# Performance work log

Hardware: AMD Instinct MI355X
Metric: run time of the kernel (lower is better)

## Reference

```python
import jax, jax.numpy as jnp
import numpy as np
import math

D_MODEL = 1024
RPN_D = 256
SUP_HW = 20  # support feature map is 20x20 -> 400 tokens


def _positional_encoding(max_len, d_model):
    pos = np.arange(max_len, dtype=np.float32)[:, None]
    div = np.exp(np.arange(0, d_model, 2, dtype=np.float32) * -(math.log(10000.0) / float(d_model)))
    pe = np.zeros((max_len, d_model), dtype=np.float32)
    pe[:, 0::2] = np.sin(pos * div)
    pe[:, 1::2] = np.cos(pos * div)
    return jnp.asarray(pe)


def setup_inputs() -> dict:
    key = jax.random.key(0)
    ks = jax.random.split(key, 6)
    B, S, H = 4, 5, 4
    fh, fw = 64, 64
    base_feat = jax.random.normal(ks[0], (B, D_MODEL, fh, fw), dtype=jnp.float32)
    support_feat = jax.random.normal(ks[1], (B, S, D_MODEL, SUP_HW, SUP_HW), dtype=jnp.float32)
    Qw = jax.random.normal(ks[2], (H, RPN_D, D_MODEL), dtype=jnp.float32) * 0.01
    Qb = jnp.zeros((H, RPN_D), dtype=jnp.float32)
    Kw = jax.random.normal(ks[3], (H, RPN_D, D_MODEL), dtype=jnp.float32) * 0.01
    Kb = jnp.zeros((H, RPN_D), dtype=jnp.float32)
    Mw = jax.random.normal(ks[4], (D_MODEL, H * D_MODEL), dtype=jnp.float32) * 0.02
    Mb = jnp.zeros((D_MODEL,), dtype=jnp.float32)
    return {"base_feat": base_feat, "support_feat": support_feat,
            "Qw": Qw, "Qb": Qb, "Kw": Kw, "Kb": Kb, "Mw": Mw, "Mb": Mb}


def reference(base_feat, support_feat, Qw, Qb, Kw, Kb, Mw, Mb):
    B, C, fh, fw = base_feat.shape
    S = support_feat.shape[1]
    H = Qw.shape[0]
    Lq = fh * fw
    Lk = SUP_HW * SUP_HW

    # support_mat: [S, B, Lk, C]  (transpose(0,1) then flatten spatial, then transpose)
    support_mat = jnp.transpose(support_feat, (1, 0, 2, 3, 4)).reshape(S, B, C, Lk)
    support_mat = jnp.transpose(support_mat, (0, 1, 3, 2))
    # query_mat: [B, Lq, C]
    query_mat = jnp.transpose(base_feat.reshape(B, C, Lq), (0, 2, 1))

    pe = _positional_encoding(400, D_MODEL)[:Lk]  # [Lk, C]
    s_mat = support_mat + pe[None, None]          # [S, B, Lk, C]

    # per-head projections (q is independent of shot, compute once)
    q = jnp.einsum('blc,hdc->hbld', query_mat, Qw) + Qb[:, None, None, :]   # [H,B,Lq,d]
    k = jnp.einsum('sbkc,hdc->hsbkd', s_mat, Kw) + Kb[:, None, None, None, :]  # [H,S,B,Lk,d]

    scores = jnp.einsum('hbld,hsbkd->hsblk', q, k) / math.sqrt(RPN_D)  # [H,S,B,Lq,Lk]
    attn = jax.nn.softmax(scores, axis=-1)
    z = jnp.einsum('hsblk,sbkc->hsblc', attn, s_mat)  # [H,S,B,Lq,C]

    # shot_mode == 'mean'
    z = jnp.mean(z, axis=1)  # [H,B,Lq,C]

    # concat heads along feature dim (head order preserved): [B,Lq,H*C]
    att = jnp.transpose(z, (1, 2, 0, 3)).reshape(B, Lq, H * C)
    att = jax.nn.relu(att @ Mw.T + Mb)  # [B,Lq,C]

    att = jnp.transpose(att, (0, 2, 1)).reshape(B, C, fh, fw)
    # attention_type == 'product'
    correlation_feat = base_feat * att
    return correlation_feat
```

## Files before the change

kernel.cpp:

```cpp
#include <hip/hip_runtime.h>
#include <stdint.h>

#define DEVI __device__ __forceinline__

typedef __attribute__((ext_vector_type(8))) short bf16x8;
typedef __attribute__((ext_vector_type(4))) float f32x4;
typedef __attribute__((ext_vector_type(4))) unsigned short us4;
typedef unsigned short u16;

constexpr int B_ = 4, S_ = 5, H_ = 4, C_ = 1024, D_ = 256;
constexpr int LQ = 4096, LK = 400, LKP = 448;

DEVI u16 f2b(float f){
  uint32_t x = __float_as_uint(f);
  uint32_t r = (x + 0x7FFFu + ((x >> 16) & 1u)) >> 16;
  return (u16)r;
}

typedef __attribute__((address_space(1))) const void ASG;
typedef __attribute__((address_space(3))) void ASL;
DEVI void gload16(const void* g, void* l){
  __builtin_amdgcn_global_load_lds((ASG*)g, (ASL*)l, 16, 0, 0);
}

__global__ __launch_bounds__(256) void k_cvt(const float* __restrict__ s, u16* __restrict__ d, int n4){
  int i = blockIdx.x*256 + threadIdx.x;
  if (i >= n4) return;
  float4 v = ((const float4*)s)[i];
  us4 o; o.x = f2b(v.x); o.y = f2b(v.y); o.z = f2b(v.z); o.w = f2b(v.w);
  *(us4*)(d + (size_t)i*4) = o;
}

__global__ __launch_bounds__(256) void k_transpose_x(const float* __restrict__ base, u16* __restrict__ Xb){
  __shared__ float t[32][33];
  int l0 = blockIdx.x*32, c0 = blockIdx.y*32, b = blockIdx.z;
  int tx = threadIdx.x & 31, ty = threadIdx.x >> 5;
  const float* src = base + ((size_t)b*C_ + c0)*LQ + l0;
  #pragma unroll
  for (int i=0;i<4;i++){ int cc = ty + i*8; t[cc][tx] = src[(size_t)cc*LQ + tx]; }
  __syncthreads();
  u16* dst = Xb + ((size_t)b*LQ + l0)*C_ + c0;
  #pragma unroll
  for (int i=0;i<4;i++){ int ll = ty + i*8; dst[(size_t)ll*C_ + tx] = f2b(t[tx][ll]); }
}

__global__ __launch_bounds__(256) void k_build_smat(const float* __restrict__ sup, u16* __restrict__ kc){
  __shared__ float t[32][33];
  int p0 = blockIdx.x*32, c0 = blockIdx.y*32;
  int s = blockIdx.z / B_, b = blockIdx.z % B_;
  int tx = threadIdx.x & 31, ty = threadIdx.x >> 5;
  const float* src = sup + ((size_t)(b*S_ + s)*C_ + c0)*LK + p0;
  #pragma unroll
  for (int i=0;i<4;i++){
    int cc = ty + i*8;
    int p = p0 + tx;
    int c = c0 + cc;
    float v = 0.f;
    if (p < LK){
      v = src[(size_t)cc*LK + tx];
      float dv = expf(-(float)(c & ~1) * (9.210340371976184f / 1024.f));
      float arg = (float)p * dv;
      v += (c & 1) ? cosf(arg) : sinf(arg);
    }
    t[cc][tx] = v;
  }
  __syncthreads();
  u16* dkc = kc + ((size_t)((s*B_ + b)*LKP + p0))*C_ + c0;
  #pragma unroll
  for (int i=0;i<4;i++){ int pp = ty + i*8; dkc[(size_t)pp*C_ + tx] = f2b(t[tx][pp]); }
}

DEVI void stage_half(const u16* P, int64_t ld, u16* dst, int wid, int r8, int s8){
  #pragma unroll
  for (int it=0; it<2; ++it){
    int ck = wid + it*8;
    gload16(P + (size_t)(ck*8 + r8)*ld + s8*8, dst + ck*512);
  }
}
DEVI bf16x8 ldsread(const u16* base, int row, int kk, int lane){
  int sl = ((kk<<2) + (lane>>4)) ^ (row & 7);
  return *(const bf16x8*)&base[row*64 + sl*8];
}

template<int CEPI, bool FIRST, bool FINAL, bool BIAS>
__global__ __launch_bounds__(512,1) void k8(
    const u16* __restrict__ A, const u16* __restrict__ Bm, void* __restrict__ Cm,
    const float* __restrict__ bias, const float* __restrict__ basep, const float* __restrict__ Mb,
    int tilesM, int64_t lda, int64_t ldb, int64_t ldc,
    int spc, int NT, int64_t aChunk, int64_t bChunk,
    int bdiv, int64_t aS0, int64_t aS1, int64_t bS0, int64_t bS1,
    int64_t cS0, int64_t cS1, int biasS0, float scale, int Nmax, int Mmax, int swz){
  __shared__ __align__(16) u16 lds[2][2][16384];
  int tid = threadIdx.x, lane = tid & 63, wid = tid >> 6;
  int bx = blockIdx.x;
  int mt, ntile;
  if (swz == 2){ int x = bx & 7, j = bx >> 3; mt = 2*x + (j >> 2); ntile = j & 3; }
  else {
    if (swz == 1) bx = (bx & 7) * (gridDim.x >> 3) + (bx >> 3);
    mt = bx % tilesM; ntile = bx / tilesM;
  }
  int z = blockIdx.y, i0 = z / bdiv, i1 = z % bdiv;
  const u16* Ab = A + i0*aS0 + i1*aS1 + (size_t)mt*256*lda;
  const u16* Bb = Bm + i0*bS0 + i1*bS1 + (size_t)ntile*256*ldb;
  int r8 = lane >> 3, s8 = (lane & 7) ^ r8;
  int wr = wid >> 2, wc = wid & 3;

  f32x4 acc[8][4];
  #pragma unroll
  for (int i=0;i<8;i++)
    #pragma unroll
    for (int j=0;j<4;j++) acc[i][j] = (f32x4){0.f,0.f,0.f,0.f};

  const u16 *ApS = Ab, *BpS = Bb; int cs = 0;
  stage_half(ApS,                   lda, &lds[0][0][0],    wid, r8, s8);
  stage_half(ApS + (size_t)128*lda, lda, &lds[0][0][8192], wid, r8, s8);
  stage_half(BpS,                   ldb, &lds[0][1][0],    wid, r8, s8);
  stage_half(BpS + (size_t)128*ldb, ldb, &lds[0][1][8192], wid, r8, s8);
  ApS += 64; BpS += 64;
  if (++cs == spc){ cs = 0; ApS += aChunk - (int64_t)spc*64; BpS += bChunk - (int64_t)spc*64; }

  for (int t = 0; t < NT; ++t){
    int cur = t & 1, nxt = cur ^ 1;
    bool pf = (t + 1 < NT);
    const u16* lA = &lds[cur][0][0];
    const u16* lB = &lds[cur][1][0];
    if (pf){
      u16* sA = &lds[nxt][0][0];
      u16* sB = &lds[nxt][1][0];
      stage_half(ApS,                   lda, sA,        wid, r8, s8);
      stage_half(ApS + (size_t)128*lda, lda, sA + 8192, wid, r8, s8);
      stage_half(BpS,                   ldb, sB,        wid, r8, s8);
      stage_half(BpS + (size_t)128*ldb, ldb, sB + 8192, wid, r8, s8);
      ApS += 64; BpS += 64;
      if (++cs == spc){ cs = 0; ApS += aChunk - (int64_t)spc*64; BpS += bChunk - (int64_t)spc*64; }
      asm volatile("s_waitcnt vmcnt(8)" ::: "memory");
    } else {
      asm volatile("s_waitcnt vmcnt(0)" ::: "memory");
    }
    asm volatile("s_barrier" ::: "memory");

    bf16x8 bfr[4][2];
    #pragma unroll
    for (int jn=0;jn<4;jn++)
      #pragma unroll
      for (int kk=0;kk<2;kk++)
        bfr[jn][kk] = ldsread(lB, wc*64 + jn*16 + (lane & 15), kk, lane);

    #pragma unroll
    for (int p = 0; p < 4; ++p){
      bf16x8 af[2][2];
      #pragma unroll
      for (int dm=0;dm<2;dm++)
        #pragma unroll
        for (int kk=0;kk<2;kk++)
          af[dm][kk] = ldsread(lA, wr*128 + (p*2+dm)*16 + (lane & 15), kk, lane);
      __builtin_amdgcn_s_setprio(1);
      #pragma unroll
      for (int dm=0;dm<2;dm++)
        #pragma unroll
        for (int jn=0;jn<4;jn++)
          #pragma unroll
          for (int kk=0;kk<2;kk++)
            acc[p*2+dm][jn] = __builtin_amdgcn_mfma_f32_16x16x32_bf16(af[dm][kk], bfr[jn][kk], acc[p*2+dm][jn], 0,0,0);
      __builtin_amdgcn_s_setprio(0);
    }
    asm volatile("s_barrier" ::: "memory");
  }

  int g = lane >> 4, c16 = lane & 15;
  if constexpr (CEPI == 0){
    u16* Cb = (u16*)Cm + i0*cS0 + i1*cS1;
    #pragma unroll
    for (int jn=0;jn<4;jn++){
      int n = ntile*256 + wc*64 + jn*16 + c16;
      if (n >= Nmax) continue;
      float bv = 0.f;
      if (BIAS) bv = bias[(size_t)i0*biasS0 + n];
      #pragma unroll
      for (int im=0;im<8;im++){
        int m = mt*256 + wr*128 + im*16 + g*4;
        if (m >= Mmax) continue;
        #pragma unroll
        for (int r=0;r<4;r++)
          Cb[(size_t)(m + r)*ldc + n] = f2b((acc[im][jn][r] + bv)*scale);
      }
    }
  } else {
    float* Cb = (float*)Cm + i0*cS0 + i1*cS1;
    const float* Bs = basep + i0*cS0 + i1*cS1;
    #pragma unroll
    for (int jn=0;jn<4;jn++){
      int n = ntile*256 + wc*64 + jn*16 + c16;
      float mbv = 0.f;
      if (FINAL) mbv = Mb[n];
      #pragma unroll
      for (int im=0;im<8;im++){
        int m = mt*256 + wr*128 + im*16 + g*4;
        float* p = Cb + (size_t)n*ldc + m;
        float4 v;
        v.x = acc[im][jn][0]; v.y = acc[im][jn][1]; v.z = acc[im][jn][2]; v.w = acc[im][jn][3];
        if (!FIRST){
          float4 old = *(const float4*)p;
          v.x += old.x; v.y += old.y; v.z += old.z; v.w += old.w;
        }
        if (FINAL){
          float4 bs = *(const float4*)(Bs + (size_t)n*ldc + m);
          v.x = bs.x * fmaxf(0.2f*v.x + mbv, 0.f);
          v.y = bs.y * fmaxf(0.2f*v.y + mbv, 0.f);
          v.z = bs.z * fmaxf(0.2f*v.z + mbv, 0.f);
          v.w = bs.w * fmaxf(0.2f*v.w + mbv, 0.f);
        }
        *(float4*)p = v;
      }
    }
  }
}

__global__ __launch_bounds__(512) void k_scores(
    const u16* __restrict__ qws, const u16* __restrict__ kws,
    u16* __restrict__ attn, int h0){
  __shared__ __align__(16) u16 lQ[128*64];
  __shared__ __align__(16) u16 lK[400*64];
  int tid = threadIdx.x, lane = tid & 63, wid = tid >> 6;
  int m0 = blockIdx.x * 128;
  int b = blockIdx.y;
  int zz = blockIdx.z;
  int s = zz % 5, h = h0 + zz / 5;
  const u16* Qp = qws + ((size_t)(h*B_ + b)*LQ + m0)*D_;
  const u16* Kp = kws + ((size_t)((h*S_ + s)*B_ + b))*((size_t)LKP*D_);
  int r8 = lane >> 3, s8 = (lane & 7) ^ r8;
  f32x4 acc[25];
  #pragma unroll
  for (int t=0;t<25;t++) acc[t] = (f32x4){0.f,0.f,0.f,0.f};
  int wm = wid * 16;
  for (int k0 = 0; k0 < 256; k0 += 64){
    __syncthreads();
    #pragma unroll
    for (int c = 0; c < 2; ++c){
      int cc = wid + c*8;
      int row = cc*8 + r8;
      gload16(Qp + (size_t)row*D_ + k0 + s8*8, &lQ[cc*512]);
    }
    for (int cc = wid; cc < 50; cc += 8){
      int row = cc*8 + r8;
      gload16(Kp + (size_t)row*D_ + k0 + s8*8, &lK[cc*512]);
    }
    __syncthreads();
    #pragma unroll
    for (int kk = 0; kk < 2; ++kk){
      int rowA = wm + (lane & 15);
      int slA = ((kk<<2) + (lane>>4)) ^ (rowA & 7);
      bf16x8 af = *(const bf16x8*)&lQ[rowA*64 + slA*8];
      #pragma unroll
      for (int t=0;t<25;t++){
        int rowB = t*16 + (lane & 15);
        int slB = ((kk<<2) + (lane>>4)) ^ (rowB & 7);
        bf16x8 bf = *(const bf16x8*)&lK[rowB*64 + slB*8];
        acc[t] = __builtin_amdgcn_mfma_f32_16x16x32_bf16(af, bf, acc[t], 0,0,0);
      }
    }
  }
  float mx[4] = {-1e30f,-1e30f,-1e30f,-1e30f};
  #pragma unroll
  for (int t=0;t<25;t++)
    #pragma unroll
    for (int r=0;r<4;r++) mx[r] = fmaxf(mx[r], acc[t][r]);
  #pragma unroll
  for (int r=0;r<4;r++){
    mx[r] = fmaxf(mx[r], __shfl_xor(mx[r], 1));
    mx[r] = fmaxf(mx[r], __shfl_xor(mx[r], 2));
    mx[r] = fmaxf(mx[r], __shfl_xor(mx[r], 4));
    mx[r] = fmaxf(mx[r], __shfl_xor(mx[r], 8));
  }
  float sm[4] = {0.f,0.f,0.f,0.f};
  #pragma unroll
  for (int t=0;t<25;t++)
    #pragma unroll
    for (int r=0;r<4;r++){ float e = __expf(acc[t][r] - mx[r]); acc[t][r] = e; sm[r] += e; }
  #pragma unroll
  for (int r=0;r<4;r++){
    sm[r] += __shfl_xor(sm[r], 1);
    sm[r] += __shfl_xor(sm[r], 2);
    sm[r] += __shfl_xor(sm[r], 4);
    sm[r] += __shfl_xor(sm[r], 8);
    sm[r] = 1.f / sm[r];
  }
  u16* ap = attn + ((size_t)((zz*B_ + b)*LQ) + m0 + wm)*LKP;
  int g = lane >> 4, c16 = lane & 15;
  #pragma unroll
  for (int t=0;t<25;t++)
    #pragma unroll
    for (int r=0;r<4;r++)
      ap[(size_t)(g*4 + r)*LKP + t*16 + c16] = f2b(acc[t][r] * sm[r]);
  for (int t = lane; t < 16*48; t += 64){
    int rr = t / 48, cp = 400 + (t % 48);
    ap[(size_t)rr*LKP + cp] = 0;
  }
}

extern "C" void kernel_launch(void* const* d_in, const int* in_sizes, int n_in,
                              void* d_out, int out_size, void* d_ws, size_t ws_size,
                              hipStream_t stream){
  const float* base = (const float*)d_in[0];
  const float* sup  = (const float*)d_in[1];
  const float* Qw   = (const float*)d_in[2];
  const float* Qb   = (const float*)d_in[3];
  const float* Kw   = (const float*)d_in[4];
  const float* Kb   = (const float*)d_in[5];
  const float* Mw   = (const float*)d_in[6];
  const float* Mb   = (const float*)d_in[7];
  float* out = (float*)d_out;
  char* ws = (char*)d_ws;

  u16* wQw = (u16*)(ws + 0);
  u16* wKw = (u16*)(ws + 2097152);
  u16* wMw = (u16*)(ws + 4194304);
  u16* wKC = (u16*)(ws + 12582912);
  u16* wK  = (u16*)(ws + 30932992);
  u16* wQ  = (u16*)(ws + 49283072);
  u16* wVt = (u16*)(ws + 82837504);

  const int GH = (ws_size >= 266338304ull) ? 2 : 1;
  const int NG = H_ / GH;
  u16* wAT = (u16*)(ws + 82837504 + (size_t)GH*18350080ull);
  u16* wXb = wAT;

  const int BIG = 1 << 30;

  k_cvt<<<1024, 256, 0, stream>>>(Qw, wQw, 262144);
  k_cvt<<<1024, 256, 0, stream>>>(Kw, wKw, 262144);
  k_cvt<<<4096, 256, 0, stream>>>(Mw, wMw, 1048576);
  k_transpose_x<<<dim3(128, 32, 4), 256, 0, stream>>>(base, wXb);
  k_build_smat<<<dim3(14, 32, 20), 256, 0, stream>>>(sup, wKC);

  k8<0,false,false,true><<<dim3(2, 80), 512, 0, stream>>>(
      wKC, wKw, wK, Kb, nullptr, nullptr,
      2, C_, C_, D_, 16, 16, 1024, 1024,
      20, 0, (int64_t)LKP*C_, (int64_t)D_*C_, 0,
      (int64_t)S_*B_*LKP*D_, (int64_t)LKP*D_, D_, 1.f, BIG, LKP, 0);

  k8<0,false,false,true><<<dim3(16, 16), 512, 0, stream>>>(
      wXb, wQw, wQ, Qb, nullptr, nullptr,
      16, C_, C_, D_, 16, 16, 1024, 1024,
      4, 0, (int64_t)LQ*C_, (int64_t)D_*C_, 0,
      (int64_t)B_*LQ*D_, (int64_t)LQ*D_, D_, 1.f/16.f, BIG, BIG, 1);

  for (int g = 0; g < NG; ++g){
    k8<0,false,false,false><<<dim3(8, GH*20), 512, 0, stream>>>(
        wMw + (size_t)(g*GH)*C_, wKC, wVt, nullptr, nullptr, nullptr,
        4, (int64_t)H_*C_, C_, LKP, 16, 16, 1024, 1024,
        20, (int64_t)C_, 0, 0, (int64_t)LKP*C_,
        (int64_t)20*C_*LKP, (int64_t)C_*LKP, 0, 1.f, LKP, BIG, 0);

    k_scores<<<dim3(32, 4, GH*5), 512, 0, stream>>>(wQ, wK, wAT, g*GH);

    if (g == 0){
      k8<1,true,false,false><<<dim3(64, 4), 512, 0, stream>>>(
          wAT, wVt, out, nullptr, base, Mb,
          16, LKP, LKP, LQ, 7, GH*35, (int64_t)B_*LQ*LKP, (int64_t)B_*C_*LKP,
          1, (int64_t)LQ*LKP, 0, (int64_t)C_*LKP, 0,
          (int64_t)C_*LQ, 0, 0, 1.f, BIG, BIG, 2);
    } else if (g == NG - 1){
      k8<1,false,true,false><<<dim3(64, 4), 512, 0, stream>>>(
          wAT, wVt, out, nullptr, base, Mb,
          16, LKP, LKP, LQ, 7, GH*35, (int64_t)B_*LQ*LKP, (int64_t)B_*C_*LKP,
          1, (int64_t)LQ*LKP, 0, (int64_t)C_*LKP, 0,
          (int64_t)C_*LQ, 0, 0, 1.f, BIG, BIG, 2);
    } else {
      k8<1,false,false,false><<<dim3(64, 4), 512, 0, stream>>>(
          wAT, wVt, out, nullptr, base, Mb,
          16, LKP, LKP, LQ, 7, GH*35, (int64_t)B_*LQ*LKP, (int64_t)B_*C_*LKP,
          1, (int64_t)LQ*LKP, 0, (int64_t)C_*LKP, 0,
          (int64_t)C_*LQ, 0, 0, 1.f, BIG, BIG, 2);
    }
  }
}
```

Baseline: 758.9 us.

## Pack attention/V along a dense KV axis, add dedicated attn-V GEMM kernel

The attention and V matrices are now packed densely along a combined shot/head KV axis (GH*5*400 rounded up to 64) instead of per-shot 448-padded chunks. This removes the chunk-stride logic and the wasted padded K-steps in the attn·V GEMM. A new k8d kernel handles that GEMM with 128x256 tiles, triple-buffered A staging and a fused residual/ReLU/product epilogue. k_scores is restructured so 8 waves split rows and KV columns, with Q read directly from global, double-buffered K in LDS and a cross-wave softmax sum through LDS. It also drops the max subtraction in softmax, which relies on scores staying small enough that exp does not overflow.

```diff
diff --git a/kernel.cpp b/kernel.cpp
--- a/kernel.cpp
+++ b/kernel.cpp
@@ -82,26 +82,23 @@
   return *(const bf16x8*)&base[row*64 + sl*8];
 }
 
-template<int CEPI, bool FIRST, bool FINAL, bool BIAS>
+template<int CEPI, bool BIAS>
 __global__ __launch_bounds__(512,1) void k8(
     const u16* __restrict__ A, const u16* __restrict__ Bm, void* __restrict__ Cm,
-    const float* __restrict__ bias, const float* __restrict__ basep, const float* __restrict__ Mb,
-    int tilesM, int64_t lda, int64_t ldb, int64_t ldc,
-    int spc, int NT, int64_t aChunk, int64_t bChunk,
+    const float* __restrict__ bias,
+    int tilesM, int64_t lda, int64_t ldb, int64_t ldc, int NT,
     int bdiv, int64_t aS0, int64_t aS1, int64_t bS0, int64_t bS1,
-    int64_t cS0, int64_t cS1, int biasS0, float scale, int Nmax, int Mmax, int swz){
+    int64_t cS0, int64_t cS1, int64_t aZ, int64_t bZ, int64_t cZ,
+    int biasS0, float scale, int Nmax, int Mmax, int swz){
   __shared__ __align__(16) u16 lds[2][2][16384];
   int tid = threadIdx.x, lane = tid & 63, wid = tid >> 6;
   int bx = blockIdx.x;
-  int mt, ntile;
-  if (swz == 2){ int x = bx & 7, j = bx >> 3; mt = 2*x + (j >> 2); ntile = j & 3; }
-  else {
-    if (swz == 1) bx = (bx & 7) * (gridDim.x >> 3) + (bx >> 3);
-    mt = bx % tilesM; ntile = bx / tilesM;
-  }
+  if (swz == 1) bx = (bx & 7) * (gridDim.x >> 3) + (bx >> 3);
+  int mt = bx % tilesM, ntile = bx / tilesM;
   int z = blockIdx.y, i0 = z / bdiv, i1 = z % bdiv;
-  const u16* Ab = A + i0*aS0 + i1*aS1 + (size_t)mt*256*lda;
-  const u16* Bb = Bm + i0*bS0 + i1*bS1 + (size_t)ntile*256*ldb;
+  int iz = blockIdx.z;
+  const u16* Ab = A + i0*aS0 + i1*aS1 + iz*aZ + (size_t)mt*256*lda;
+  const u16* Bb = Bm + i0*bS0 + i1*bS1 + iz*bZ + (size_t)ntile*256*ldb;
   int r8 = lane >> 3, s8 = (lane & 7) ^ r8;
   int wr = wid >> 2, wc = wid & 3;
 
@@ -111,13 +108,12 @@
     #pragma unroll
     for (int j=0;j<4;j++) acc[i][j] = (f32x4){0.f,0.f,0.f,0.f};
 
-  const u16 *ApS = Ab, *BpS = Bb; int cs = 0;
+  const u16 *ApS = Ab, *BpS = Bb;
   stage_half(ApS,                   lda, &lds[0][0][0],    wid, r8, s8);
   stage_half(ApS + (size_t)128*lda, lda, &lds[0][0][8192], wid, r8, s8);
   stage_half(BpS,                   ldb, &lds[0][1][0],    wid, r8, s8);
   stage_half(BpS + (size_t)128*ldb, ldb, &lds[0][1][8192], wid, r8, s8);
   ApS += 64; BpS += 64;
-  if (++cs == spc){ cs = 0; ApS += aChunk - (int64_t)spc*64; BpS += bChunk - (int64_t)spc*64; }
 
   for (int t = 0; t < NT; ++t){
     int cur = t & 1, nxt = cur ^ 1;
@@ -132,7 +128,6 @@
       stage_half(BpS,                   ldb, sB,        wid, r8, s8);
       stage_half(BpS + (size_t)128*ldb, ldb, sB + 8192, wid, r8, s8);
       ApS += 64; BpS += 64;
-      if (++cs == spc){ cs = 0; ApS += aChunk - (int64_t)spc*64; BpS += bChunk - (int64_t)spc*64; }
       asm volatile("s_waitcnt vmcnt(8)" ::: "memory");
     } else {
       asm volatile("s_waitcnt vmcnt(0)" ::: "memory");
@@ -168,59 +163,134 @@
   }
 
   int g = lane >> 4, c16 = lane & 15;
-  if constexpr (CEPI == 0){
-    u16* Cb = (u16*)Cm + i0*cS0 + i1*cS1;
-    #pragma unroll
-    for (int jn=0;jn<4;jn++){
-      int n = ntile*256 + wc*64 + jn*16 + c16;
-      if (n >= Nmax) continue;
-      float bv = 0.f;
-      if (BIAS) bv = bias[(size_t)i0*biasS0 + n];
-      #pragma unroll
-      for (int im=0;im<8;im++){
-        int m = mt*256 + wr*128 + im*16 + g*4;
-        if (m >= Mmax) continue;
+  u16* Cb = (u16*)Cm + i0*cS0 + i1*cS1 + iz*cZ;
+  #pragma unroll
+  for (int jn=0;jn<4;jn++){
+    int n = ntile*256 + wc*64 + jn*16 + c16;
+    if (n >= Nmax) continue;
+    float bv = 0.f;
+    if (BIAS) bv = bias[(size_t)i0*biasS0 + n];
+    #pragma unroll
+    for (int im=0;im<8;im++){
+      int m = mt*256 + wr*128 + im*16 + g*4;
+      if (m >= Mmax) continue;
+      #pragma unroll
+      for (int r=0;r<4;r++)
+        Cb[(size_t)(m + r)*ldc + n] = f2b((acc[im][jn][r] + bv)*scale);
+    }
+  }
+}
+
+template<bool FIRST, bool FINAL>
+__global__ __launch_bounds__(512,1) void k8d(
+    const u16* __restrict__ A, const u16* __restrict__ Bm, float* __restrict__ Cm,
+    const float* __restrict__ basep, const float* __restrict__ Mb,
+    int KVP, int NT){
+  __shared__ __align__(16) u16 lA[3][8192];
+  __shared__ __align__(16) u16 lB[2][16384];
+  int tid = threadIdx.x, lane = tid & 63, wid = tid >> 6;
+  int x = blockIdx.x & 7, jj = blockIdx.x >> 3;
+  int mt = x*4 + (jj >> 2), nt = jj & 3;
+  int b = blockIdx.y;
+  const u16* Ab = A + ((size_t)b*LQ + (size_t)mt*128)*KVP;
+  const u16* Bb = Bm + ((size_t)b*C_ + (size_t)nt*256)*KVP;
+  int r8 = lane >> 3, s8 = (lane & 7) ^ r8;
+  int wr = wid >> 2, wc = wid & 3;
+
+  f32x4 acc[4][4];
+  #pragma unroll
+  for (int i=0;i<4;i++)
+    #pragma unroll
+    for (int j=0;j<4;j++) acc[i][j] = (f32x4){0.f,0.f,0.f,0.f};
+
+  const u16 *Bp = Bb, *Ap = Ab;
+  stage_half(Bp,                   KVP, lB[0],        wid, r8, s8);
+  stage_half(Bp + (size_t)128*KVP, KVP, lB[0] + 8192, wid, r8, s8);
+  Bp += 64;
+  stage_half(Ap, KVP, lA[0], wid, r8, s8); Ap += 64;
+  stage_half(Ap, KVP, lA[1], wid, r8, s8); Ap += 64;
+
+  int ia = 0, ia2 = 2, ib = 0;
+  for (int t = 0; t < NT; ++t){
+    const u16* lAc = lA[ia];
+    const u16* lBc = lB[ib];
+    if (t + 1 < NT){
+      u16* dB = lB[ib ^ 1];
+      stage_half(Bp,                   KVP, dB,        wid, r8, s8);
+      stage_half(Bp + (size_t)128*KVP, KVP, dB + 8192, wid, r8, s8);
+      Bp += 64;
+    }
+    if (t + 2 < NT){
+      stage_half(Ap, KVP, lA[ia2], wid, r8, s8);
+      Ap += 64;
+    }
+    if (t + 2 < NT)      asm volatile("s_waitcnt vmcnt(8)" ::: "memory");
+    else if (t + 1 < NT) asm volatile("s_waitcnt vmcnt(6)" ::: "memory");
+    else                 asm volatile("s_waitcnt vmcnt(0)" ::: "memory");
+    asm volatile("s_barrier" ::: "memory");
+
+    bf16x8 bfr[4][2], af[4][2];
+    #pragma unroll
+    for (int jn=0;jn<4;jn++)
+      #pragma unroll
+      for (int kk=0;kk<2;kk++)
+        bfr[jn][kk] = ldsread(lBc, wc*64 + jn*16 + (lane & 15), kk, lane);
+    #pragma unroll
+    for (int im=0;im<4;im++)
+      #pragma unroll
+      for (int kk=0;kk<2;kk++)
+        af[im][kk] = ldsread(lAc, wr*64 + im*16 + (lane & 15), kk, lane);
+    __builtin_amdgcn_s_setprio(1);
+    #pragma unroll
+    for (int im=0;im<4;im++)
+      #pragma unroll
+      for (int jn=0;jn<4;jn++)
         #pragma unroll
-        for (int r=0;r<4;r++)
-          Cb[(size_t)(m + r)*ldc + n] = f2b((acc[im][jn][r] + bv)*scale);
-      }
-    }
-  } else {
-    float* Cb = (float*)Cm + i0*cS0 + i1*cS1;
-    const float* Bs = basep + i0*cS0 + i1*cS1;
-    #pragma unroll
-    for (int jn=0;jn<4;jn++){
-      int n = ntile*256 + wc*64 + jn*16 + c16;
-      float mbv = 0.f;
-      if (FINAL) mbv = Mb[n];
-      #pragma unroll
-      for (int im=0;im<8;im++){
-        int m = mt*256 + wr*128 + im*16 + g*4;
-        float* p = Cb + (size_t)n*ldc + m;
-        float4 v;
-        v.x = acc[im][jn][0]; v.y = acc[im][jn][1]; v.z = acc[im][jn][2]; v.w = acc[im][jn][3];
-        if (!FIRST){
-          float4 old = *(const float4*)p;
-          v.x += old.x; v.y += old.y; v.z += old.z; v.w += old.w;
-        }
-        if (FINAL){
-          float4 bs = *(const float4*)(Bs + (size_t)n*ldc + m);
-          v.x = bs.x * fmaxf(0.2f*v.x + mbv, 0.f);
-          v.y = bs.y * fmaxf(0.2f*v.y + mbv, 0.f);
-          v.z = bs.z * fmaxf(0.2f*v.z + mbv, 0.f);
-          v.w = bs.w * fmaxf(0.2f*v.w + mbv, 0.f);
-        }
-        *(float4*)p = v;
-      }
+        for (int kk=0;kk<2;kk++)
+          acc[im][jn] = __builtin_amdgcn_mfma_f32_16x16x32_bf16(af[im][kk], bfr[jn][kk], acc[im][jn], 0,0,0);
+    __builtin_amdgcn_s_setprio(0);
+    asm volatile("s_barrier" ::: "memory");
+    ia = (ia + 1 == 3) ? 0 : ia + 1;
+    ia2 = (ia2 + 1 == 3) ? 0 : ia2 + 1;
+    ib ^= 1;
+  }
+
+  int g = lane >> 4, c16 = lane & 15;
+  float* Cb = Cm + (size_t)b*C_*LQ;
+  const float* Bs = basep + (size_t)b*C_*LQ;
+  #pragma unroll
+  for (int jn=0;jn<4;jn++){
+    int n = nt*256 + wc*64 + jn*16 + c16;
+    float mbv = 0.f;
+    if (FINAL) mbv = Mb[n];
+    #pragma unroll
+    for (int im=0;im<4;im++){
+      int m = mt*128 + wr*64 + im*16 + g*4;
+      float* p = Cb + (size_t)n*LQ + m;
+      float4 v;
+      v.x = acc[im][jn][0]; v.y = acc[im][jn][1]; v.z = acc[im][jn][2]; v.w = acc[im][jn][3];
+      if (!FIRST){
+        float4 old = *(const float4*)p;
+        v.x += old.x; v.y += old.y; v.z += old.z; v.w += old.w;
+      }
+      if (FINAL){
+        float4 bs = *(const float4*)(Bs + (size_t)n*LQ + m);
+        v.x = bs.x * fmaxf(0.2f*v.x + mbv, 0.f);
+        v.y = bs.y * fmaxf(0.2f*v.y + mbv, 0.f);
+        v.z = bs.z * fmaxf(0.2f*v.z + mbv, 0.f);
+        v.w = bs.w * fmaxf(0.2f*v.w + mbv, 0.f);
+      }
+      *(float4*)p = v;
     }
   }
 }
 
 __global__ __launch_bounds__(512) void k_scores(
     const u16* __restrict__ qws, const u16* __restrict__ kws,
-    u16* __restrict__ attn, int h0){
-  __shared__ __align__(16) u16 lQ[128*64];
-  __shared__ __align__(16) u16 lK[400*64];
+    u16* __restrict__ attn, int h0, int KVP, int padw, int nz){
+  __shared__ __align__(16) u16 lK[2][448*64];
+  __shared__ float red[128][4];
+  __shared__ float rsum[128];
   int tid = threadIdx.x, lane = tid & 63, wid = tid >> 6;
   int m0 = blockIdx.x * 128;
   int b = blockIdx.y;
@@ -229,72 +299,110 @@
   const u16* Qp = qws + ((size_t)(h*B_ + b)*LQ + m0)*D_;
   const u16* Kp = kws + ((size_t)((h*S_ + s)*B_ + b))*((size_t)LKP*D_);
   int r8 = lane >> 3, s8 = (lane & 7) ^ r8;
-  f32x4 acc[25];
-  #pragma unroll
-  for (int t=0;t<25;t++) acc[t] = (f32x4){0.f,0.f,0.f,0.f};
-  int wm = wid * 16;
-  for (int k0 = 0; k0 < 256; k0 += 64){
-    __syncthreads();
-    #pragma unroll
-    for (int c = 0; c < 2; ++c){
-      int cc = wid + c*8;
-      int row = cc*8 + r8;
-      gload16(Qp + (size_t)row*D_ + k0 + s8*8, &lQ[cc*512]);
-    }
-    for (int cc = wid; cc < 50; cc += 8){
-      int row = cc*8 + r8;
-      gload16(Kp + (size_t)row*D_ + k0 + s8*8, &lK[cc*512]);
-    }
-    __syncthreads();
-    #pragma unroll
-    for (int kk = 0; kk < 2; ++kk){
-      int rowA = wm + (lane & 15);
-      int slA = ((kk<<2) + (lane>>4)) ^ (rowA & 7);
-      bf16x8 af = *(const bf16x8*)&lQ[rowA*64 + slA*8];
-      #pragma unroll
-      for (int t=0;t<25;t++){
-        int rowB = t*16 + (lane & 15);
-        int slB = ((kk<<2) + (lane>>4)) ^ (rowB & 7);
-        bf16x8 bf = *(const bf16x8*)&lK[rowB*64 + slB*8];
-        acc[t] = __builtin_amdgcn_mfma_f32_16x16x32_bf16(af, bf, acc[t], 0,0,0);
-      }
-    }
-  }
-  float mx[4] = {-1e30f,-1e30f,-1e30f,-1e30f};
-  #pragma unroll
-  for (int t=0;t<25;t++)
-    #pragma unroll
-    for (int r=0;r<4;r++) mx[r] = fmaxf(mx[r], acc[t][r]);
-  #pragma unroll
-  for (int r=0;r<4;r++){
-    mx[r] = fmaxf(mx[r], __shfl_xor(mx[r], 1));
-    mx[r] = fmaxf(mx[r], __shfl_xor(mx[r], 2));
-    mx[r] = fmaxf(mx[r], __shfl_xor(mx[r], 4));
-    mx[r] = fmaxf(mx[r], __shfl_xor(mx[r], 8));
-  }
-  float sm[4] = {0.f,0.f,0.f,0.f};
-  #pragma unroll
-  for (int t=0;t<25;t++)
-    #pragma unroll
-    for (int r=0;r<4;r++){ float e = __expf(acc[t][r] - mx[r]); acc[t][r] = e; sm[r] += e; }
-  #pragma unroll
-  for (int r=0;r<4;r++){
-    sm[r] += __shfl_xor(sm[r], 1);
-    sm[r] += __shfl_xor(sm[r], 2);
-    sm[r] += __shfl_xor(sm[r], 4);
-    sm[r] += __shfl_xor(sm[r], 8);
-    sm[r] = 1.f / sm[r];
-  }
-  u16* ap = attn + ((size_t)((zz*B_ + b)*LQ) + m0 + wm)*LKP;
-  int g = lane >> 4, c16 = lane & 15;
-  #pragma unroll
-  for (int t=0;t<25;t++)
-    #pragma unroll
-    for (int r=0;r<4;r++)
-      ap[(size_t)(g*4 + r)*LKP + t*16 + c16] = f2b(acc[t][r] * sm[r]);
-  for (int t = lane; t < 16*48; t += 64){
-    int rr = t / 48, cp = 400 + (t % 48);
-    ap[(size_t)rr*LKP + cp] = 0;
+  int c16 = lane & 15, g = lane >> 4;
+  int wm2 = wid >> 2, wkv = wid & 3;
+
+  f32x4 acc[4][7];
+  #pragma unroll
+  for (int m=0;m<4;m++)
+    #pragma unroll
+    for (int t=0;t<7;t++) acc[m][t] = (f32x4){0.f,0.f,0.f,0.f};
+
+  #pragma unroll
+  for (int i=0;i<7;i++){
+    int ck = wid + i*8;
+    gload16(Kp + (size_t)(ck*8 + r8)*D_ + s8*8, &lK[0][ck*512]);
+  }
+
+  for (int t = 0; t < 4; ++t){
+    int k0 = t*64;
+    bf16x8 af[4][2];
+    #pragma unroll
+    for (int m=0;m<4;m++)
+      #pragma unroll
+      for (int kk=0;kk<2;kk++){
+        int row = wm2*64 + m*16 + c16;
+        af[m][kk] = *(const bf16x8*)(Qp + (size_t)row*D_ + k0 + kk*32 + g*8);
+      }
+    if (t + 1 < 4){
+      #pragma unroll
+      for (int i=0;i<7;i++){
+        int ck = wid + i*8;
+        gload16(Kp + (size_t)(ck*8 + r8)*D_ + (k0 + 64) + s8*8, &lK[(t+1)&1][ck*512]);
+      }
+      asm volatile("s_waitcnt vmcnt(15)" ::: "memory");
+    } else {
+      asm volatile("s_waitcnt vmcnt(8)" ::: "memory");
+    }
+    asm volatile("s_barrier" ::: "memory");
+    const u16* lKc = &lK[t & 1][0];
+    __builtin_amdgcn_s_setprio(1);
+    #pragma unroll
+    for (int tt=0;tt<7;tt++)
+      #pragma unroll
+      for (int kk=0;kk<2;kk++){
+        bf16x8 bf = ldsread(lKc, wkv*112 + tt*16 + c16, kk, lane);
+        #pragma unroll
+        for (int m=0;m<4;m++)
+          acc[m][tt] = __builtin_amdgcn_mfma_f32_16x16x32_bf16(af[m][kk], bf, acc[m][tt], 0,0,0);
+      }
+    __builtin_amdgcn_s_setprio(0);
+    asm volatile("s_barrier" ::: "memory");
+  }
+
+  int tmax = (wkv == 3) ? 4 : 7;
+  float psum[4][4];
+  #pragma unroll
+  for (int m=0;m<4;m++)
+    #pragma unroll
+    for (int r=0;r<4;r++) psum[m][r] = 0.f;
+  for (int tt=0; tt<tmax; ++tt)
+    #pragma unroll
+    for (int m=0;m<4;m++)
+      #pragma unroll
+      for (int r=0;r<4;r++){
+        float e = __expf(acc[m][tt][r]);
+        acc[m][tt][r] = e;
+        psum[m][r] += e;
+      }
+  #pragma unroll
+  for (int m=0;m<4;m++)
+    #pragma unroll
+    for (int r=0;r<4;r++){
+      psum[m][r] += __shfl_xor(psum[m][r], 1);
+      psum[m][r] += __shfl_xor(psum[m][r], 2);
+      psum[m][r] += __shfl_xor(psum[m][r], 4);
+      psum[m][r] += __shfl_xor(psum[m][r], 8);
+    }
+  if (c16 == 0){
+    #pragma unroll
+    for (int m=0;m<4;m++)
+      #pragma unroll
+      for (int r=0;r<4;r++)
+        red[wm2*64 + m*16 + g*4 + r][wkv] = psum[m][r];
+  }
+  __syncthreads();
+  if (tid < 128) rsum[tid] = 1.f / (red[tid][0] + red[tid][1] + red[tid][2] + red[tid][3]);
+  __syncthreads();
+
+  u16* ap = attn + ((size_t)b*LQ + m0)*KVP + (size_t)zz*400;
+  for (int m=0;m<4;m++)
+    #pragma unroll
+    for (int r=0;r<4;r++){
+      int rowl = wm2*64 + m*16 + g*4 + r;
+      float rs = rsum[rowl];
+      for (int tt=0; tt<tmax; ++tt){
+        int col = wkv*112 + tt*16 + c16;
+        ap[(size_t)rowl*KVP + col] = f2b(acc[m][tt][r] * rs);
+      }
+    }
+  if (zz == nz - 1 && padw > 0){
+    u16* base2 = attn + ((size_t)b*LQ + m0)*KVP + (KVP - padw);
+    int total = 128 * padw;
+    for (int i = tid; i < total; i += 512){
+      int rr = i / padw, cc = i % padw;
+      base2[(size_t)rr*KVP + cc] = 0;
+    }
   }
 }
 
@@ -312,6 +420,13 @@
   float* out = (float*)d_out;
   char* ws = (char*)d_ws;
 
+  const int GH = (ws_size >= 247988224ull) ? 2 : 1;
+  const int NG = H_ / GH;
+  const int NZ = GH * 5;
+  const int KVP = (NZ*400 + 63) & ~63;
+  const int NT = KVP / 64;
+  const int PADW = KVP - NZ*400;
+
   u16* wQw = (u16*)(ws + 0);
   u16* wKw = (u16*)(ws + 2097152);
   u16* wMw = (u16*)(ws + 4194304);
@@ -319,10 +434,7 @@
   u16* wK  = (u16*)(ws + 30932992);
   u16* wQ  = (u16*)(ws + 49283072);
   u16* wVt = (u16*)(ws + 82837504);
-
-  const int GH = (ws_size >= 266338304ull) ? 2 : 1;
-  const int NG = H_ / GH;
-  u16* wAT = (u16*)(ws + 82837504 + (size_t)GH*18350080ull);
+  u16* wAT = (u16*)(ws + 82837504 + (size_t)B_*C_*KVP*2);
   u16* wXb = wAT;
 
   const int BIG = 1 << 30;
@@ -333,45 +445,36 @@
   k_transpose_x<<<dim3(128, 32, 4), 256, 0, stream>>>(base, wXb);
   k_build_smat<<<dim3(14, 32, 20), 256, 0, stream>>>(sup, wKC);
 
-  k8<0,false,false,true><<<dim3(2, 80), 512, 0, stream>>>(
-      wKC, wKw, wK, Kb, nullptr, nullptr,
-      2, C_, C_, D_, 16, 16, 1024, 1024,
+  k8<0,true><<<dim3(2, 80, 1), 512, 0, stream>>>(
+      wKC, wKw, wK, Kb,
+      2, C_, C_, D_, 16,
       20, 0, (int64_t)LKP*C_, (int64_t)D_*C_, 0,
-      (int64_t)S_*B_*LKP*D_, (int64_t)LKP*D_, D_, 1.f, BIG, LKP, 0);
-
-  k8<0,false,false,true><<<dim3(16, 16), 512, 0, stream>>>(
-      wXb, wQw, wQ, Qb, nullptr, nullptr,
-      16, C_, C_, D_, 16, 16, 1024, 1024,
+      (int64_t)S_*B_*LKP*D_, (int64_t)LKP*D_, 0, 0, 0,
+      D_, 1.f, BIG, LKP, 0);
+
+  k8<0,true><<<dim3(16, 16, 1), 512, 0, stream>>>(
+      wXb, wQw, wQ, Qb,
+      16, C_, C_, D_, 16,
       4, 0, (int64_t)LQ*C_, (int64_t)D_*C_, 0,
-      (int64_t)B_*LQ*D_, (int64_t)LQ*D_, D_, 1.f/16.f, BIG, BIG, 1);
+      (int64_t)B_*LQ*D_, (int64_t)LQ*D_, 0, 0, 0,
+      D_, 1.f/16.f, BIG, BIG, 1);
 
   for (int g = 0; g < NG; ++g){
-    k8<0,false,false,false><<<dim3(8, GH*20), 512, 0, stream>>>(
-        wMw + (size_t)(g*GH)*C_, wKC, wVt, nullptr, nullptr, nullptr,
-        4, (int64_t)H_*C_, C_, LKP, 16, 16, 1024, 1024,
-        20, (int64_t)C_, 0, 0, (int64_t)LKP*C_,
-        (int64_t)20*C_*LKP, (int64_t)C_*LKP, 0, 1.f, LKP, BIG, 0);
-
-    k_scores<<<dim3(32, 4, GH*5), 512, 0, stream>>>(wQ, wK, wAT, g*GH);
-
-    if (g == 0){
-      k8<1,true,false,false><<<dim3(64, 4), 512, 0, stream>>>(
-          wAT, wVt, out, nullptr, base, Mb,
-          16, LKP, LKP, LQ, 7, GH*35, (int64_t)B_*LQ*LKP, (int64_t)B_*C_*LKP,
-          1, (int64_t)LQ*LKP, 0, (int64_t)C_*LKP, 0,
-          (int64_t)C_*LQ, 0, 0, 1.f, BIG, BIG, 2);
+    k8<0,false><<<dim3(8, NZ, 4), 512, 0, stream>>>(
+        wMw + (size_t)(g*GH)*C_, wKC, wVt, nullptr,
+        4, (int64_t)H_*C_, C_, KVP, 16,
+        5, (int64_t)C_, 0, 0, (int64_t)B_*LKP*C_,
+        2000, 400, 0, (int64_t)LKP*C_, (int64_t)C_*KVP,
+        0, 1.f, 400, BIG, 0);
+
+    k_scores<<<dim3(32, 4, NZ), 512, 0, stream>>>(wQ, wK, wAT, g*GH, KVP, PADW, NZ);
+
+    if (g == 0 && NG > 1){
+      k8d<true,false><<<dim3(128, 4), 512, 0, stream>>>(wAT, wVt, out, base, Mb, KVP, NT);
     } else if (g == NG - 1){
-      k8<1,false,true,false><<<dim3(64, 4), 512, 0, stream>>>(
-          wAT, wVt, out, nullptr, base, Mb,
-          16, LKP, LKP, LQ, 7, GH*35, (int64_t)B_*LQ*LKP, (int64_t)B_*C_*LKP,
-          1, (int64_t)LQ*LKP, 0, (int64_t)C_*LKP, 0,
-          (int64_t)C_*LQ, 0, 0, 1.f, BIG, BIG, 2);
+      k8d<false,true><<<dim3(128, 4), 512, 0, stream>>>(wAT, wVt, out, base, Mb, KVP, NT);
     } else {
-      k8<1,false,false,false><<<dim3(64, 4), 512, 0, stream>>>(
-          wAT, wVt, out, nullptr, base, Mb,
-          16, LKP, LKP, LQ, 7, GH*35, (int64_t)B_*LQ*LKP, (int64_t)B_*C_*LKP,
-          1, (int64_t)LQ*LKP, 0, (int64_t)C_*LKP, 0,
-          (int64_t)C_*LQ, 0, 0, 1.f, BIG, BIG, 2);
-    }
-  }
-}
+      k8d<false,false><<<dim3(128, 4), 512, 0, stream>>>(wAT, wVt, out, base, Mb, KVP, NT);
+    }
+  }
+}
```

Measured after the change: 1.960 ms. 158% more time.

## Pack shot/head attention chunks contiguously along K and stagger B-tile prefetch

Applied to the files above, without the earlier changes.

Attention probabilities and the V^T matrix now place all shots and heads of a group contiguously along the reduction dimension, padded once to a multiple of 64 instead of padding each 400-wide chunk to 448. This removes the per-chunk pointer jumps in the GEMM and cuts wasted padded K iterations, so the big attn×V GEMM does less work. The B-operand prefetch is also split and issued between MFMA phases to overlap loads with compute, with the wait count adjusted. Risks are wait-count correctness with the staggered loads, and if NG is 1 the first-pass epilogue path changes.

```diff
diff --git a/kernel.cpp b/kernel.cpp
--- a/kernel.cpp
+++ b/kernel.cpp
@@ -86,10 +86,10 @@
 __global__ __launch_bounds__(512,1) void k8(
     const u16* __restrict__ A, const u16* __restrict__ Bm, void* __restrict__ Cm,
     const float* __restrict__ bias, const float* __restrict__ basep, const float* __restrict__ Mb,
-    int tilesM, int64_t lda, int64_t ldb, int64_t ldc,
-    int spc, int NT, int64_t aChunk, int64_t bChunk,
+    int tilesM, int64_t lda, int64_t ldb, int64_t ldc, int NT,
     int bdiv, int64_t aS0, int64_t aS1, int64_t bS0, int64_t bS1,
-    int64_t cS0, int64_t cS1, int biasS0, float scale, int Nmax, int Mmax, int swz){
+    int64_t cS0, int64_t cS1, int64_t aZ, int64_t bZ, int64_t cZ,
+    int biasS0, float scale, int Nmax, int Mmax, int swz){
   __shared__ __align__(16) u16 lds[2][2][16384];
   int tid = threadIdx.x, lane = tid & 63, wid = tid >> 6;
   int bx = blockIdx.x;
@@ -100,8 +100,9 @@
     mt = bx % tilesM; ntile = bx / tilesM;
   }
   int z = blockIdx.y, i0 = z / bdiv, i1 = z % bdiv;
-  const u16* Ab = A + i0*aS0 + i1*aS1 + (size_t)mt*256*lda;
-  const u16* Bb = Bm + i0*bS0 + i1*bS1 + (size_t)ntile*256*ldb;
+  int iz = blockIdx.z;
+  const u16* Ab = A + i0*aS0 + i1*aS1 + iz*aZ + (size_t)mt*256*lda;
+  const u16* Bb = Bm + i0*bS0 + i1*bS1 + iz*bZ + (size_t)ntile*256*ldb;
   int r8 = lane >> 3, s8 = (lane & 7) ^ r8;
   int wr = wid >> 2, wc = wid & 3;
 
@@ -111,29 +112,24 @@
     #pragma unroll
     for (int j=0;j<4;j++) acc[i][j] = (f32x4){0.f,0.f,0.f,0.f};
 
-  const u16 *ApS = Ab, *BpS = Bb; int cs = 0;
+  const u16 *ApS = Ab, *BpS = Bb;
   stage_half(ApS,                   lda, &lds[0][0][0],    wid, r8, s8);
   stage_half(ApS + (size_t)128*lda, lda, &lds[0][0][8192], wid, r8, s8);
   stage_half(BpS,                   ldb, &lds[0][1][0],    wid, r8, s8);
   stage_half(BpS + (size_t)128*ldb, ldb, &lds[0][1][8192], wid, r8, s8);
   ApS += 64; BpS += 64;
-  if (++cs == spc){ cs = 0; ApS += aChunk - (int64_t)spc*64; BpS += bChunk - (int64_t)spc*64; }
 
   for (int t = 0; t < NT; ++t){
     int cur = t & 1, nxt = cur ^ 1;
     bool pf = (t + 1 < NT);
     const u16* lA = &lds[cur][0][0];
     const u16* lB = &lds[cur][1][0];
+    u16* sA = &lds[nxt][0][0];
+    u16* sB = &lds[nxt][1][0];
     if (pf){
-      u16* sA = &lds[nxt][0][0];
-      u16* sB = &lds[nxt][1][0];
       stage_half(ApS,                   lda, sA,        wid, r8, s8);
       stage_half(ApS + (size_t)128*lda, lda, sA + 8192, wid, r8, s8);
-      stage_half(BpS,                   ldb, sB,        wid, r8, s8);
-      stage_half(BpS + (size_t)128*ldb, ldb, sB + 8192, wid, r8, s8);
-      ApS += 64; BpS += 64;
-      if (++cs == spc){ cs = 0; ApS += aChunk - (int64_t)spc*64; BpS += bChunk - (int64_t)spc*64; }
-      asm volatile("s_waitcnt vmcnt(8)" ::: "memory");
+      asm volatile("s_waitcnt vmcnt(4)" ::: "memory");
     } else {
       asm volatile("s_waitcnt vmcnt(0)" ::: "memory");
     }
@@ -163,13 +159,16 @@
           for (int kk=0;kk<2;kk++)
             acc[p*2+dm][jn] = __builtin_amdgcn_mfma_f32_16x16x32_bf16(af[dm][kk], bfr[jn][kk], acc[p*2+dm][jn], 0,0,0);
       __builtin_amdgcn_s_setprio(0);
+      if (p == 0 && pf) stage_half(BpS,                   ldb, sB,        wid, r8, s8);
+      if (p == 1 && pf) stage_half(BpS + (size_t)128*ldb, ldb, sB + 8192, wid, r8, s8);
     }
     asm volatile("s_barrier" ::: "memory");
+    if (pf){ ApS += 64; BpS += 64; }
   }
 
   int g = lane >> 4, c16 = lane & 15;
   if constexpr (CEPI == 0){
-    u16* Cb = (u16*)Cm + i0*cS0 + i1*cS1;
+    u16* Cb = (u16*)Cm + i0*cS0 + i1*cS1 + iz*cZ;
     #pragma unroll
     for (int jn=0;jn<4;jn++){
       int n = ntile*256 + wc*64 + jn*16 + c16;
@@ -186,8 +185,8 @@
       }
     }
   } else {
-    float* Cb = (float*)Cm + i0*cS0 + i1*cS1;
-    const float* Bs = basep + i0*cS0 + i1*cS1;
+    float* Cb = (float*)Cm + i0*cS0 + i1*cS1 + iz*cZ;
+    const float* Bs = basep + i0*cS0 + i1*cS1 + iz*cZ;
     #pragma unroll
     for (int jn=0;jn<4;jn++){
       int n = ntile*256 + wc*64 + jn*16 + c16;
@@ -218,7 +217,7 @@
 
 __global__ __launch_bounds__(512) void k_scores(
     const u16* __restrict__ qws, const u16* __restrict__ kws,
-    u16* __restrict__ attn, int h0){
+    u16* __restrict__ attn, int h0, int KVP, int padw, int nz){
   __shared__ __align__(16) u16 lQ[128*64];
   __shared__ __align__(16) u16 lK[400*64];
   int tid = threadIdx.x, lane = tid & 63, wid = tid >> 6;
@@ -285,16 +284,20 @@
     sm[r] += __shfl_xor(sm[r], 8);
     sm[r] = 1.f / sm[r];
   }
-  u16* ap = attn + ((size_t)((zz*B_ + b)*LQ) + m0 + wm)*LKP;
+  u16* ap = attn + ((size_t)b*LQ + m0 + wm)*KVP + (size_t)zz*400;
   int g = lane >> 4, c16 = lane & 15;
   #pragma unroll
   for (int t=0;t<25;t++)
     #pragma unroll
     for (int r=0;r<4;r++)
-      ap[(size_t)(g*4 + r)*LKP + t*16 + c16] = f2b(acc[t][r] * sm[r]);
-  for (int t = lane; t < 16*48; t += 64){
-    int rr = t / 48, cp = 400 + (t % 48);
-    ap[(size_t)rr*LKP + cp] = 0;
+      ap[(size_t)(g*4 + r)*KVP + t*16 + c16] = f2b(acc[t][r] * sm[r]);
+  if (zz == nz - 1 && padw > 0){
+    u16* base2 = attn + ((size_t)b*LQ + m0)*KVP + (KVP - padw);
+    int total = 128 * padw;
+    for (int i = tid; i < total; i += 512){
+      int rr = i / padw, cc = i % padw;
+      base2[(size_t)rr*KVP + cc] = 0;
+    }
   }
 }
 
@@ -312,6 +315,13 @@
   float* out = (float*)d_out;
   char* ws = (char*)d_ws;
 
+  const int GH = (ws_size >= 247988224ull) ? 2 : 1;
+  const int NG = H_ / GH;
+  const int NZ = GH * 5;
+  const int KVP = (NZ*400 + 63) & ~63;
+  const int NT = KVP / 64;
+  const int PADW = KVP - NZ*400;
+
   u16* wQw = (u16*)(ws + 0);
   u16* wKw = (u16*)(ws + 2097152);
   u16* wMw = (u16*)(ws + 4194304);
@@ -319,10 +329,7 @@
   u16* wK  = (u16*)(ws + 30932992);
   u16* wQ  = (u16*)(ws + 49283072);
   u16* wVt = (u16*)(ws + 82837504);
-
-  const int GH = (ws_size >= 266338304ull) ? 2 : 1;
-  const int NG = H_ / GH;
-  u16* wAT = (u16*)(ws + 82837504 + (size_t)GH*18350080ull);
+  u16* wAT = (u16*)(ws + 82837504 + (size_t)B_*C_*KVP*2);
   u16* wXb = wAT;
 
   const int BIG = 1 << 30;
@@ -333,45 +340,51 @@
   k_transpose_x<<<dim3(128, 32, 4), 256, 0, stream>>>(base, wXb);
   k_build_smat<<<dim3(14, 32, 20), 256, 0, stream>>>(sup, wKC);
 
-  k8<0,false,false,true><<<dim3(2, 80), 512, 0, stream>>>(
+  k8<0,false,false,true><<<dim3(2, 80, 1), 512, 0, stream>>>(
       wKC, wKw, wK, Kb, nullptr, nullptr,
-      2, C_, C_, D_, 16, 16, 1024, 1024,
+      2, C_, C_, D_, 16,
       20, 0, (int64_t)LKP*C_, (int64_t)D_*C_, 0,
-      (int64_t)S_*B_*LKP*D_, (int64_t)LKP*D_, D_, 1.f, BIG, LKP, 0);
-
-  k8<0,false,false,true><<<dim3(16, 16), 512, 0, stream>>>(
+      (int64_t)S_*B_*LKP*D_, (int64_t)LKP*D_, 0, 0, 0,
+      D_, 1.f, BIG, LKP, 0);
+
+  k8<0,false,false,true><<<dim3(16, 16, 1), 512, 0, stream>>>(
       wXb, wQw, wQ, Qb, nullptr, nullptr,
-      16, C_, C_, D_, 16, 16, 1024, 1024,
+      16, C_, C_, D_, 16,
       4, 0, (int64_t)LQ*C_, (int64_t)D_*C_, 0,
-      (int64_t)B_*LQ*D_, (int64_t)LQ*D_, D_, 1.f/16.f, BIG, BIG, 1);
+      (int64_t)B_*LQ*D_, (int64_t)LQ*D_, 0, 0, 0,
+      D_, 1.f/16.f, BIG, BIG, 1);
 
   for (int g = 0; g < NG; ++g){
-    k8<0,false,false,false><<<dim3(8, GH*20), 512, 0, stream>>>(
+    k8<0,false,false,false><<<dim3(8, NZ, 4), 512, 0, stream>>>(
         wMw + (size_t)(g*GH)*C_, wKC, wVt, nullptr, nullptr, nullptr,
-        4, (int64_t)H_*C_, C_, LKP, 16, 16, 1024, 1024,
-        20, (int64_t)C_, 0, 0, (int64_t)LKP*C_,
-        (int64_t)20*C_*LKP, (int64_t)C_*LKP, 0, 1.f, LKP, BIG, 0);
-
-    k_scores<<<dim3(32, 4, GH*5), 512, 0, stream>>>(wQ, wK, wAT, g*GH);
-
-    if (g == 0){
-      k8<1,true,false,false><<<dim3(64, 4), 512, 0, stream>>>(
+        4, (int64_t)H_*C_, C_, KVP, 16,
+        5, (int64_t)C_, 0, 0, (int64_t)B_*LKP*C_,
+        2000, 400, 0, (int64_t)LKP*C_, (int64_t)C_*KVP,
+        0, 1.f, 400, BIG, 0);
+
+    k_scores<<<dim3(32, 4, NZ), 512, 0, stream>>>(wQ, wK, wAT, g*GH, KVP, PADW, NZ);
+
+    if (g == 0 && NG > 1){
+      k8<1,true,false,false><<<dim3(64, 4, 1), 512, 0, stream>>>(
           wAT, wVt, out, nullptr, base, Mb,
-          16, LKP, LKP, LQ, 7, GH*35, (int64_t)B_*LQ*LKP, (int64_t)B_*C_*LKP,
-          1, (int64_t)LQ*LKP, 0, (int64_t)C_*LKP, 0,
-          (int64_t)C_*LQ, 0, 0, 1.f, BIG, BIG, 2);
+          16, KVP, KVP, LQ, NT,
+          1, (int64_t)LQ*KVP, 0, (int64_t)C_*KVP, 0,
+          (int64_t)C_*LQ, 0, 0, 0, 0,
+          0, 1.f, BIG, BIG, 2);
     } else if (g == NG - 1){
-      k8<1,false,true,false><<<dim3(64, 4), 512, 0, stream>>>(
+      k8<1,false,true,false><<<dim3(64, 4, 1), 512, 0, stream>>>(
           wAT, wVt, out, nullptr, base, Mb,
-          16, LKP, LKP, LQ, 7, GH*35, (int64_t)B_*LQ*LKP, (int64_t)B_*C_*LKP,
-          1, (int64_t)LQ*LKP, 0, (int64_t)C_*LKP, 0,
-          (int64_t)C_*LQ, 0, 0, 1.f, BIG, BIG, 2);
+          16, KVP, KVP, LQ, NT,
+          1, (int64_t)LQ*KVP, 0, (int64_t)C_*KVP, 0,
+          (int64_t)C_*LQ, 0, 0, 0, 0,
+          0, 1.f, BIG, BIG, 2);
     } else {
-      k8<1,false,false,false><<<dim3(64, 4), 512, 0, stream>>>(
+      k8<1,false,false,false><<<dim3(64, 4, 1), 512, 0, stream>>>(
           wAT, wVt, out, nullptr, base, Mb,
-          16, LKP, LKP, LQ, 7, GH*35, (int64_t)B_*LQ*LKP, (int64_t)B_*C_*LKP,
-          1, (int64_t)LQ*LKP, 0, (int64_t)C_*LKP, 0,
-          (int64_t)C_*LQ, 0, 0, 1.f, BIG, BIG, 2);
-    }
-  }
-}
+          16, KVP, KVP, LQ, NT,
+          1, (int64_t)LQ*KVP, 0, (int64_t)C_*KVP, 0,
+          (int64_t)C_*LQ, 0, 0, 0, 0,
+          0, 1.f, BIG, BIG, 2);
+    }
+  }
+}
```

Result: faster. 701.8 us (-7.5%).
